# Kernel tuning notes

Hardware: AMD Instinct MI355X
Metric: run time of the kernel (lower is better)

The kernel has to match this reference:

```python
import jax, jax.numpy as jnp
import numpy as np

D = 1152      # hidden_size
H = 16        # num_heads
DH = D // H   # head_dim = 72
NCHUNK = 8    # images
L = 1024      # tokens per image (32x32 patches)
S = NCHUNK * L


def rotate_half(x):
    x1, x2 = jnp.split(x, 2, axis=-1)
    return jnp.concatenate([-x2, x1], axis=-1)


def setup_inputs() -> dict:
    key = jax.random.key(0)
    k0, k1, k2, k3, k4 = jax.random.split(key, 5)
    hidden_states = jax.random.normal(k0, (S, D), dtype=jnp.float32)
    qkv_w = jax.random.normal(k1, (3 * D, D), dtype=jnp.float32) * 0.02
    qkv_b = jax.random.normal(k2, (3 * D,), dtype=jnp.float32) * 0.02
    proj_w = jax.random.normal(k3, (D, D), dtype=jnp.float32) * 0.02
    proj_b = jax.random.normal(k4, (D,), dtype=jnp.float32) * 0.02
    # vision RoPE tables: [S, head_dim] with duplicated half-frequencies
    pos = jnp.arange(S, dtype=jnp.float32)
    inv_freq = 1.0 / (10000.0 ** (jnp.arange(0, DH, 2, dtype=jnp.float32) / DH))
    freqs = jnp.outer(pos, inv_freq)              # [S, DH//2]
    emb = jnp.concatenate([freqs, freqs], -1)     # [S, DH]
    cos, sin = jnp.cos(emb), jnp.sin(emb)
    cu_seqlens = jnp.arange(NCHUNK + 1, dtype=jnp.int32) * L
    return dict(hidden_states=hidden_states, cos=cos, sin=sin,
                qkv_w=qkv_w, qkv_b=qkv_b, proj_w=proj_w, proj_b=proj_b,
                cu_seqlens=cu_seqlens)


def reference(hidden_states, cos, sin, qkv_w, qkv_b, proj_w, proj_b, cu_seqlens):
    seq = hidden_states.shape[0]
    num_heads = H
    head_dim = qkv_w.shape[0] // (3 * num_heads)
    # fused QKV projection (torch Linear: x @ W^T + b)
    qkv = hidden_states @ qkv_w.T + qkv_b                 # [S, 3D]
    qkv = qkv.reshape(seq, 3, num_heads, head_dim)
    q, k, v = qkv[:, 0], qkv[:, 1], qkv[:, 2]             # [S, H, DH]
    # RoPE in fp32, broadcast cos/sin over heads
    c = cos[:, None, :].astype(jnp.float32)
    s = sin[:, None, :].astype(jnp.float32)
    qf, kf = q.astype(jnp.float32), k.astype(jnp.float32)
    q = (qf * c + rotate_half(qf) * s).astype(q.dtype)
    k = (kf * c + rotate_half(kf) * s).astype(k.dtype)
    # cu_seqlens defines equal-length segments -> vectorize over chunks
    cu = np.asarray(cu_seqlens)
    chunk = int(cu[1] - cu[0])
    n = seq // chunk
    qc = q.reshape(n, chunk, num_heads, head_dim)
    kc = k.reshape(n, chunk, num_heads, head_dim)
    vc = v.reshape(n, chunk, num_heads, head_dim)
    scale = head_dim ** -0.5
    attn = jnp.einsum('nqhd,nkhd->nhqk', qc, kc) * scale  # [n,H,L,L]
    attn = jax.nn.softmax(attn.astype(jnp.float32), axis=-1).astype(q.dtype)
    out = jnp.einsum('nhqk,nkhd->nqhd', attn, vc)         # [n,L,H,DH]
    out = out.reshape(seq, num_heads * head_dim)
    return out @ proj_w.T + proj_b
```

## Files before the change

kernel.cpp:

```cpp
#include <hip/hip_runtime.h>
#include <stdint.h>

typedef unsigned short ushort_t;
typedef short bf16x8 __attribute__((ext_vector_type(8)));
typedef float f32x4 __attribute__((ext_vector_type(4)));
typedef ushort_t us2 __attribute__((ext_vector_type(2)));
typedef ushort_t us4 __attribute__((ext_vector_type(4)));
typedef ushort_t us8 __attribute__((ext_vector_type(8)));

__device__ __forceinline__ float b2f(ushort_t u) {
    union { unsigned int i; float f; } v; v.i = ((unsigned int)u) << 16; return v.f;
}
__device__ __forceinline__ ushort_t f2b(float f) {
    union { float f; unsigned int i; } v; v.f = f;
    unsigned int r = v.i + 0x7fffu + ((v.i >> 16) & 1u);
    return (ushort_t)(r >> 16);
}

typedef __attribute__((address_space(3))) unsigned int lds_u32;
typedef __attribute__((address_space(1))) const unsigned int gbl_u32;

__device__ __forceinline__ void gload_lds16(const void* g, void* l) {
    __builtin_amdgcn_global_load_lds((gbl_u32*)g, (lds_u32*)l, 16, 0, 0);
}

__global__ void cvt_f32_bf16(const float* __restrict__ src, ushort_t* __restrict__ dst, int n8)
{
    const int i = blockIdx.x * 256 + threadIdx.x;
    if (i >= n8) return;
    f32x4 a = *(const f32x4*)&src[i * 8];
    f32x4 b = *(const f32x4*)&src[i * 8 + 4];
    us8 o;
#pragma unroll
    for (int j = 0; j < 4; j++) { o[j] = f2b(a[j]); o[j + 4] = f2b(b[j]); }
    *(us8*)&dst[i * 8] = o;
}

template <bool OUT_F32>
__global__ __launch_bounds__(256, 2) void gemm_bt_bias(
    const ushort_t* __restrict__ A, const ushort_t* __restrict__ B,
    const float* __restrict__ bias, void* __restrict__ Cv,
    int M, int N, int K)
{
    __shared__ short As[128 * 32];
    __shared__ short Bs[128 * 32];
    const int t = threadIdx.x;
    const int lane = t & 63, w = t >> 6;
    const int qd = lane >> 4, ln = lane & 15;
    const int wm = w >> 1, wn = w & 1;
    const int m0 = blockIdx.y * 128, n0 = blockIdx.x * 128;

    f32x4 acc[4][4];
#pragma unroll
    for (int i = 0; i < 4; i++)
#pragma unroll
        for (int j = 0; j < 4; j++) acc[i][j] = (f32x4){0.f, 0.f, 0.f, 0.f};

    const int rowA = t >> 2, c16 = t & 3;
    const ushort_t* gA  = A + (size_t)(m0 + rowA) * K + c16 * 8;
    const ushort_t* gA2 = A + (size_t)(m0 + 64 + rowA) * K + c16 * 8;
    const ushort_t* gB  = B + (size_t)(n0 + rowA) * K + c16 * 8;
    const ushort_t* gB2 = B + (size_t)(n0 + 64 + rowA) * K + c16 * 8;
    short* lA  = &As[t * 8];
    short* lA2 = &As[(t + 256) * 8];
    short* lB  = &Bs[t * 8];
    short* lB2 = &Bs[(t + 256) * 8];

    for (int k0 = 0; k0 < K; k0 += 32) {
        __syncthreads();
        gload_lds16(gA + k0, lA);
        gload_lds16(gA2 + k0, lA2);
        gload_lds16(gB + k0, lB);
        gload_lds16(gB2 + k0, lB2);
        __syncthreads();

        bf16x8 af[4], bfv[4];
#pragma unroll
        for (int i = 0; i < 4; i++)
            af[i] = *(const bf16x8*)&As[(wm * 64 + i * 16 + ln) * 32 + qd * 8];
#pragma unroll
        for (int j = 0; j < 4; j++)
            bfv[j] = *(const bf16x8*)&Bs[(wn * 64 + j * 16 + ln) * 32 + qd * 8];
#pragma unroll
        for (int i = 0; i < 4; i++)
#pragma unroll
            for (int j = 0; j < 4; j++)
                acc[i][j] = __builtin_amdgcn_mfma_f32_16x16x32_bf16(
                    af[i], bfv[j], acc[i][j], 0, 0, 0);
    }

#pragma unroll
    for (int j = 0; j < 4; j++) {
        const int col = n0 + wn * 64 + j * 16 + ln;
        const float bv = bias[col];
#pragma unroll
        for (int i = 0; i < 4; i++) {
#pragma unroll
            for (int r = 0; r < 4; r++) {
                const int row = m0 + wm * 64 + i * 16 + qd * 4 + r;
                const float val = acc[i][j][r] + bv;
                if (OUT_F32) ((float*)Cv)[(size_t)row * N + col] = val;
                else         ((ushort_t*)Cv)[(size_t)row * N + col] = f2b(val);
            }
        }
    }
}

__global__ void rope_qk(ushort_t* __restrict__ qkv,
                        const float* __restrict__ cosb,
                        const float* __restrict__ sinb,
                        ushort_t* __restrict__ kb)
{
    const int idx = blockIdx.x * 256 + threadIdx.x;
    const int d0c = idx % 9;
    const int h = (idx / 9) & 15;
    const int s = idx / 144;
    const int d0 = d0c * 4;
    const int n = s >> 10, l = s & 1023;
    const size_t src = (size_t)s * 3456 + h * 72;
    const size_t dstrow = ((size_t)(n * 16 + h) * 1024 + l) * 128;

    f32x4 c1 = *(const f32x4*)&cosb[s * 72 + d0];
    f32x4 c2 = *(const f32x4*)&cosb[s * 72 + d0 + 36];
    f32x4 s1 = *(const f32x4*)&sinb[s * 72 + d0];
    f32x4 s2 = *(const f32x4*)&sinb[s * 72 + d0 + 36];

    {
        us4 x1 = *(const us4*)&qkv[src + d0];
        us4 x2 = *(const us4*)&qkv[src + d0 + 36];
        us4 o1, o2;
#pragma unroll
        for (int j = 0; j < 4; j++) {
            float a = b2f(x1[j]), b = b2f(x2[j]);
            o1[j] = f2b(a * c1[j] - b * s1[j]);
            o2[j] = f2b(b * c2[j] + a * s2[j]);
        }
        *(us4*)&qkv[src + d0] = o1;
        *(us4*)&qkv[src + d0 + 36] = o2;
    }
    {
        us4 x1 = *(const us4*)&qkv[src + 1152 + d0];
        us4 x2 = *(const us4*)&qkv[src + 1152 + d0 + 36];
        us4 o1, o2;
#pragma unroll
        for (int j = 0; j < 4; j++) {
            float a = b2f(x1[j]), b = b2f(x2[j]);
            o1[j] = f2b(a * c1[j] - b * s1[j]);
            o2[j] = f2b(b * c2[j] + a * s2[j]);
        }
        *(us4*)&kb[dstrow + d0] = o1;
        *(us4*)&kb[dstrow + d0 + 36] = o2;
    }
    if (d0c < 7) {
        us8 z = (us8){0, 0, 0, 0, 0, 0, 0, 0};
        *(us8*)&kb[dstrow + 72 + d0c * 8] = z;
    }
}

__global__ void v_transpose(const ushort_t* __restrict__ qkv, ushort_t* __restrict__ vt)
{
    __shared__ short T[64 * 80];
    const int t = threadIdx.x;
    const int nh = blockIdx.x >> 4, kvb = blockIdx.x & 15;
    const int h = nh & 15, n = nh >> 4;
    const int s0 = n * 1024 + kvb * 64;

#pragma unroll
    for (int i = 0; i < 3; i++) {
        int c = t + i * 256;
        if (c < 576) {
            int row = c / 9, off = (c % 9) * 8;
            *(us8*)&T[row * 80 + off] =
                *(const us8*)&qkv[(size_t)(s0 + row) * 3456 + 2304 + h * 72 + off];
        }
    }
    __syncthreads();

#pragma unroll
    for (int i = 0; i < 3; i++) {
        int c = t + i * 256;
        if (c < 640) {
            int d = c >> 3, kc = c & 7;
            us8 o;
            if (d < 72) {
#pragma unroll
                for (int j = 0; j < 8; j++) o[j] = (ushort_t)T[(kc * 8 + j) * 80 + d];
            } else {
                o = (us8){0, 0, 0, 0, 0, 0, 0, 0};
            }
            *(us8*)&vt[((size_t)nh * 80 + d) * 1024 + kvb * 64 + kc * 8] = o;
        }
    }
}

__global__ __launch_bounds__(256, 2) void flash_attn(
    const ushort_t* __restrict__ qkv, const ushort_t* __restrict__ kb,
    const ushort_t* __restrict__ vt, ushort_t* __restrict__ ob)
{
    __shared__ short Ks[2][64 * 128];
    __shared__ short VtS[2][80 * 64];
    __shared__ short Ps[4][32 * 72];

    const int t = threadIdx.x;
    const int lane = t & 63, w = t >> 6;
    const int qd = lane >> 4, ln = lane & 15;
    const int lnx = ln & 7;
    const int nh = blockIdx.x >> 3, qt = blockIdx.x & 7;
    const int q0 = qt * 128;
    const int h = nh & 15, n = nh >> 4;
    const float scale = 0.11785113019775793f;

    const ushort_t* kbase = kb + (size_t)nh * 1024 * 128;
    const ushort_t* vbase = vt + (size_t)nh * 80 * 1024;

    bf16x8 qf[2][3];
    {
        const ushort_t* qsrc = qkv + (size_t)(n * 1024 + q0 + w * 32) * 3456 + h * 72;
#pragma unroll
        for (int im = 0; im < 2; im++)
#pragma unroll
            for (int ks = 0; ks < 3; ks++)
                qf[im][ks] = *(const bf16x8*)&qsrc[(size_t)(im * 16 + ln) * 3456 + ks * 32 + qd * 8];
    }

#pragma unroll
    for (int i = 0; i < 4; i++) {
        int c = t + i * 256, r = c >> 4, kc = c & 15;
        gload_lds16(kbase + (size_t)r * 128 + (kc ^ (r & 7)) * 8, &Ks[0][c * 8]);
    }
#pragma unroll
    for (int i = 0; i < 3; i++) {
        int c = t + i * 256;
        if (c < 640) {
            int d = c >> 3, kc = c & 7;
            gload_lds16(vbase + (size_t)d * 1024 + (kc ^ (d & 7)) * 8, &VtS[0][c * 8]);
        }
    }

    float l_lane[2][4];
    f32x4 acc_o[2][5];
#pragma unroll
    for (int im = 0; im < 2; im++) {
#pragma unroll
        for (int r = 0; r < 4; r++) l_lane[im][r] = 0.f;
#pragma unroll
        for (int jn = 0; jn < 5; jn++) acc_o[im][jn] = (f32x4){0.f, 0.f, 0.f, 0.f};
    }

    for (int it = 0; it < 16; it++) {
        __syncthreads();

        if (it < 15) {
            const int nb = (it + 1) & 1;
            const ushort_t* knext = kbase + (size_t)(it + 1) * 8192;
#pragma unroll
            for (int i = 0; i < 4; i++) {
                int c = t + i * 256, r = c >> 4, kc = c & 15;
                gload_lds16(knext + (size_t)r * 128 + (kc ^ (r & 7)) * 8, &Ks[nb][c * 8]);
            }
            const ushort_t* vnext = vbase + (it + 1) * 64;
#pragma unroll
            for (int i = 0; i < 3; i++) {
                int c = t + i * 256;
                if (c < 640) {
                    int d = c >> 3, kc = c & 7;
                    gload_lds16(vnext + (size_t)d * 1024 + (kc ^ (d & 7)) * 8, &VtS[nb][c * 8]);
                }
            }
        }

        const short* KsB = Ks[it & 1];
        const short* VtB = VtS[it & 1];

        f32x4 sc[2][4];
#pragma unroll
        for (int im = 0; im < 2; im++)
#pragma unroll
            for (int jk = 0; jk < 4; jk++) sc[im][jk] = (f32x4){0.f, 0.f, 0.f, 0.f};
#pragma unroll
        for (int ks = 0; ks < 3; ks++) {
            const int m = ks * 4 + qd;
#pragma unroll
            for (int jk = 0; jk < 4; jk++) {
                bf16x8 bfr = *(const bf16x8*)&KsB[(jk * 16 + ln) * 128 + (m ^ lnx) * 8];
                sc[0][jk] = __builtin_amdgcn_mfma_f32_16x16x32_bf16(qf[0][ks], bfr, sc[0][jk], 0, 0, 0);
                sc[1][jk] = __builtin_amdgcn_mfma_f32_16x16x32_bf16(qf[1][ks], bfr, sc[1][jk], 0, 0, 0);
            }
        }

#pragma unroll
        for (int im = 0; im < 2; im++) {
#pragma unroll
            for (int r = 0; r < 4; r++) {
                float p0 = __expf(sc[im][0][r] * scale);
                float p1 = __expf(sc[im][1][r] * scale);
                float p2 = __expf(sc[im][2][r] * scale);
                float p3 = __expf(sc[im][3][r] * scale);
                l_lane[im][r] += (p0 + p1) + (p2 + p3);
                short* pd = &Ps[w][(im * 16 + qd * 4 + r) * 72 + ln];
                pd[0]  = (short)f2b(p0);
                pd[16] = (short)f2b(p1);
                pd[32] = (short)f2b(p2);
                pd[48] = (short)f2b(p3);
            }
        }

#pragma unroll
        for (int ks = 0; ks < 2; ks++) {
            const int m = ks * 4 + qd;
            bf16x8 p0f = *(const bf16x8*)&Ps[w][(ln) * 72 + ks * 32 + qd * 8];
            bf16x8 p1f = *(const bf16x8*)&Ps[w][(16 + ln) * 72 + ks * 32 + qd * 8];
#pragma unroll
            for (int jn = 0; jn < 5; jn++) {
                bf16x8 vf = *(const bf16x8*)&VtB[(jn * 16 + ln) * 64 + (m ^ lnx) * 8];
                acc_o[0][jn] = __builtin_amdgcn_mfma_f32_16x16x32_bf16(p0f, vf, acc_o[0][jn], 0, 0, 0);
                acc_o[1][jn] = __builtin_amdgcn_mfma_f32_16x16x32_bf16(p1f, vf, acc_o[1][jn], 0, 0, 0);
            }
        }
    }

    const size_t obase = ((size_t)(n * 1024 + q0)) * 1152 + h * 72;
#pragma unroll
    for (int im = 0; im < 2; im++) {
#pragma unroll
        for (int r = 0; r < 4; r++) {
            float l = l_lane[im][r];
            l += __shfl_xor(l, 1);
            l += __shfl_xor(l, 2);
            l += __shfl_xor(l, 4);
            l += __shfl_xor(l, 8);
            const float inv = 1.0f / l;
            const int rowl = w * 32 + im * 16 + qd * 4 + r;
#pragma unroll
            for (int jn = 0; jn < 5; jn++) {
                const int d = jn * 16 + ln;
                if (d < 72)
                    ob[obase + (size_t)rowl * 1152 + d] = f2b(acc_o[im][jn][r] * inv);
            }
        }
    }
}

extern "C" void kernel_launch(void* const* d_in, const int* in_sizes, int n_in,
                              void* d_out, int out_size, void* d_ws, size_t ws_size,
                              hipStream_t stream)
{
    const float* hs     = (const float*)d_in[0];
    const float* cosb   = (const float*)d_in[1];
    const float* sinb   = (const float*)d_in[2];
    const float* qkv_w  = (const float*)d_in[3];
    const float* qkv_b  = (const float*)d_in[4];
    const float* proj_w = (const float*)d_in[5];
    const float* proj_b = (const float*)d_in[6];

    char* ws = (char*)d_ws;
    ushort_t* hs_bf   = (ushort_t*)(ws);
    ushort_t* attn    = (ushort_t*)(ws);
    ushort_t* qkvw_bf = (ushort_t*)(ws + 18874368);
    ushort_t* projw_bf= (ushort_t*)(ws + 26836992);
    ushort_t* qkv_tmp = (ushort_t*)(ws + 29491200);
    ushort_t* k_buf   = (ushort_t*)(ws + 86114304);
    ushort_t* v_t     = (ushort_t*)(ws + 119668736);
    float*    out     = (float*)d_out;

    cvt_f32_bf16<<<4608, 256, 0, stream>>>(hs, hs_bf, 9437184 / 8);
    cvt_f32_bf16<<<1944, 256, 0, stream>>>(qkv_w, qkvw_bf, 3981312 / 8);
    cvt_f32_bf16<<<648, 256, 0, stream>>>(proj_w, projw_bf, 1327104 / 8);

    gemm_bt_bias<false><<<dim3(27, 64), 256, 0, stream>>>(hs_bf, qkvw_bf, qkv_b, qkv_tmp, 8192, 3456, 1152);
    rope_qk<<<4608, 256, 0, stream>>>(qkv_tmp, cosb, sinb, k_buf);
    v_transpose<<<2048, 256, 0, stream>>>(qkv_tmp, v_t);
    flash_attn<<<1024, 256, 0, stream>>>(qkv_tmp, k_buf, v_t, attn);
    gemm_bt_bias<true><<<dim3(9, 64), 256, 0, stream>>>(attn, projw_bf, proj_b, out, 8192, 1152, 1152);
}
```

Baseline: 369.3 us.

## Double-buffer GEMM LDS tiles with XOR swizzle and stage epilogue through LDS

The QKV and output-projection GEMM now double-buffers its LDS tiles, prefetching the next K-slice with global_load_lds while the current one feeds the MFMAs. This drops one barrier per iteration and hides load latency. The LDS column index is XOR-swizzled to cut bank conflicts on fragment reads. The epilogue stages results through LDS so global stores are coalesced 16-byte writes instead of scattered scalar stores, and launch bounds ask for 4 blocks per CU. The cost is twice the LDS per block, and there is a possible race if the async LDS write of the next buffer is not waited on before it is read.

Measured after the change: 364.1 us. Within noise of the previous version (-1.4%).

```diff
diff --git a/kernel.cpp b/kernel.cpp
--- a/kernel.cpp
+++ b/kernel.cpp
@@ -37,18 +37,19 @@
 }
 
 template <bool OUT_F32>
-__global__ __launch_bounds__(256, 2) void gemm_bt_bias(
+__global__ __launch_bounds__(256, 4) void gemm_bt_bias(
     const ushort_t* __restrict__ A, const ushort_t* __restrict__ B,
     const float* __restrict__ bias, void* __restrict__ Cv,
     int M, int N, int K)
 {
-    __shared__ short As[128 * 32];
-    __shared__ short Bs[128 * 32];
+    __shared__ short Sm[16384];
+
     const int t = threadIdx.x;
     const int lane = t & 63, w = t >> 6;
     const int qd = lane >> 4, ln = lane & 15;
     const int wm = w >> 1, wn = w & 1;
     const int m0 = blockIdx.y * 128, n0 = blockIdx.x * 128;
+    const int KITER = K >> 5;
 
     f32x4 acc[4][4];
 #pragma unroll
@@ -56,31 +57,41 @@
 #pragma unroll
         for (int j = 0; j < 4; j++) acc[i][j] = (f32x4){0.f, 0.f, 0.f, 0.f};
 
-    const int rowA = t >> 2, c16 = t & 3;
-    const ushort_t* gA  = A + (size_t)(m0 + rowA) * K + c16 * 8;
-    const ushort_t* gA2 = A + (size_t)(m0 + 64 + rowA) * K + c16 * 8;
-    const ushort_t* gB  = B + (size_t)(n0 + rowA) * K + c16 * 8;
-    const ushort_t* gB2 = B + (size_t)(n0 + 64 + rowA) * K + c16 * 8;
-    short* lA  = &As[t * 8];
-    short* lA2 = &As[(t + 256) * 8];
-    short* lB  = &Bs[t * 8];
-    short* lB2 = &Bs[(t + 256) * 8];
-
-    for (int k0 = 0; k0 < K; k0 += 32) {
+    const int rA = t >> 2;
+    const int colSw = ((t & 3) ^ (rA & 3)) * 8;
+    const ushort_t* gA  = A + (size_t)(m0 + rA) * K + colSw;
+    const ushort_t* gA2 = A + (size_t)(m0 + 64 + rA) * K + colSw;
+    const ushort_t* gB  = B + (size_t)(n0 + rA) * K + colSw;
+    const ushort_t* gB2 = B + (size_t)(n0 + 64 + rA) * K + colSw;
+
+    gload_lds16(gA,  Sm + t * 8);
+    gload_lds16(gA2, Sm + (t + 256) * 8);
+    gload_lds16(gB,  Sm + 8192 + t * 8);
+    gload_lds16(gB2, Sm + 8192 + (t + 256) * 8);
+
+    const int pc = (qd ^ (ln & 3)) * 8;
+
+    for (int kt = 0; kt < KITER; kt++) {
         __syncthreads();
-        gload_lds16(gA + k0, lA);
-        gload_lds16(gA2 + k0, lA2);
-        gload_lds16(gB + k0, lB);
-        gload_lds16(gB2 + k0, lB2);
-        __syncthreads();
+        if (kt + 1 < KITER) {
+            const int k1 = (kt + 1) << 5;
+            const int nbo = ((kt + 1) & 1) * 4096;
+            gload_lds16(gA + k1,  Sm + nbo + t * 8);
+            gload_lds16(gA2 + k1, Sm + nbo + (t + 256) * 8);
+            gload_lds16(gB + k1,  Sm + 8192 + nbo + t * 8);
+            gload_lds16(gB2 + k1, Sm + 8192 + nbo + (t + 256) * 8);
+        }
+        const int cbo = (kt & 1) * 4096;
+        const short* AsB = Sm + cbo;
+        const short* BsB = Sm + 8192 + cbo;
 
         bf16x8 af[4], bfv[4];
 #pragma unroll
         for (int i = 0; i < 4; i++)
-            af[i] = *(const bf16x8*)&As[(wm * 64 + i * 16 + ln) * 32 + qd * 8];
+            af[i] = *(const bf16x8*)&AsB[(wm * 64 + i * 16 + ln) * 32 + pc];
 #pragma unroll
         for (int j = 0; j < 4; j++)
-            bfv[j] = *(const bf16x8*)&Bs[(wn * 64 + j * 16 + ln) * 32 + qd * 8];
+            bfv[j] = *(const bf16x8*)&BsB[(wn * 64 + j * 16 + ln) * 32 + pc];
 #pragma unroll
         for (int i = 0; i < 4; i++)
 #pragma unroll
@@ -89,18 +100,52 @@
                     af[i], bfv[j], acc[i][j], 0, 0, 0);
     }
 
-#pragma unroll
-    for (int j = 0; j < 4; j++) {
-        const int col = n0 + wn * 64 + j * 16 + ln;
-        const float bv = bias[col];
-#pragma unroll
-        for (int i = 0; i < 4; i++) {
-#pragma unroll
-            for (int r = 0; r < 4; r++) {
-                const int row = m0 + wm * 64 + i * 16 + qd * 4 + r;
-                const float val = acc[i][j][r] + bv;
-                if (OUT_F32) ((float*)Cv)[(size_t)row * N + col] = val;
-                else         ((ushort_t*)Cv)[(size_t)row * N + col] = f2b(val);
+    float bv[4];
+#pragma unroll
+    for (int j = 0; j < 4; j++) bv[j] = bias[n0 + wn * 64 + j * 16 + ln];
+
+    if (!OUT_F32) {
+        __syncthreads();
+        ushort_t* Ct = (ushort_t*)Cv;
+#pragma unroll
+        for (int i = 0; i < 4; i++)
+#pragma unroll
+            for (int j = 0; j < 4; j++)
+#pragma unroll
+                for (int r = 0; r < 4; r++)
+                    Sm[(wm * 64 + i * 16 + qd * 4 + r) * 128 + wn * 64 + j * 16 + ln] =
+                        (short)f2b(acc[i][j][r] + bv[j]);
+        __syncthreads();
+#pragma unroll
+        for (int q = 0; q < 8; q++) {
+            const int c = t + q * 256;
+            const int row = c >> 4, cc = c & 15;
+            *(us8*)&Ct[(size_t)(m0 + row) * N + n0 + cc * 8] =
+                *(const us8*)&Sm[row * 128 + cc * 8];
+        }
+    } else {
+        float* Ct = (float*)Cv;
+        float* Cf = (float*)Sm;
+#pragma unroll
+        for (int p = 0; p < 2; p++) {
+            __syncthreads();
+            if (wm == p) {
+#pragma unroll
+                for (int i = 0; i < 4; i++)
+#pragma unroll
+                    for (int j = 0; j < 4; j++)
+#pragma unroll
+                        for (int r = 0; r < 4; r++)
+                            Cf[(i * 16 + qd * 4 + r) * 128 + wn * 64 + j * 16 + ln] =
+                                acc[i][j][r] + bv[j];
+            }
+            __syncthreads();
+#pragma unroll
+            for (int q = 0; q < 8; q++) {
+                const int c = t + q * 256;
+                const int row = c >> 5, cc = c & 31;
+                *(f32x4*)&Ct[(size_t)(m0 + p * 64 + row) * N + n0 + cc * 4] =
+                    *(const f32x4*)&Cf[row * 128 + cc * 4];
             }
         }
     }
```
